# Performance work log

Hardware: AMD Instinct MI355X
Metric: run time of the kernel (lower is better)

## Reference

```python
import jax, jax.numpy as jnp
import numpy as np

B, H, S, D = 4, 32, 2048, 128  # batch, heads, seq_len, d_head
D_MODEL = H * D


def setup_inputs() -> dict:
    key = jax.random.key(0)
    ks = jax.random.split(key, 6)
    return {
        "query_states": jax.random.normal(ks[0], (B, H, S, D), dtype=jnp.float32),
        "key_states": jax.random.normal(ks[1], (B, H, S, D), dtype=jnp.float32),
        "value_states": jax.random.normal(ks[2], (B, H, S, D), dtype=jnp.float32),
        "local_attn_outputs": jax.random.normal(ks[3], (B, H, S, D), dtype=jnp.float32),
        "balance_factors": jax.random.normal(ks[4], (H,), dtype=jnp.float32),
        "w_o": jax.random.normal(ks[5], (D_MODEL, D_MODEL), dtype=jnp.float32) / np.sqrt(D_MODEL),
    }


def reference(query_states, key_states, value_states, local_attn_outputs, balance_factors, w_o):
    # --- compressive memory from keys/values (elu+1 feature map) ---
    phi_k = jax.nn.elu(key_states) + 1.0                                  # [B,H,S,D]
    memory = jnp.einsum("bhsk,bhsv->bhkv", phi_k, value_states)           # [B,H,D,D]
    normalization = jnp.sum(phi_k, axis=2)                                # [B,H,D]

    # --- retrieval with query feature map, normalized ---
    phi_q = jax.nn.elu(query_states) + 1.0                                # [B,H,S,D]
    retrieved = jnp.einsum("bhsk,bhkv->bhsv", phi_q, memory)              # [B,H,S,D]
    denom = jnp.einsum("bhsk,bhk->bhs", phi_q, normalization)             # [B,H,S]
    retrieved = retrieved / denom[..., None]

    # --- sigmoid-gated combine of global (memory) and local attention ---
    gw = jax.nn.sigmoid(balance_factors)[None, :, None, None]             # global weights
    lw = jax.nn.sigmoid(1.0 - balance_factors)[None, :, None, None]      # local weights
    attn = gw * retrieved + lw * local_attn_outputs                       # [B,H,S,D]

    # [B,H,S,D] -> [B,S,H*D]
    attn = jnp.transpose(attn, (0, 2, 1, 3)).reshape(B, S, H * D)
    # o_proj: bias-free Linear, y = x @ W^T
    return attn @ w_o.T
```

## Files before the change

### kernel.cpp

```cpp
#include <hip/hip_runtime.h>
#include <hip/hip_bf16.h>

#define B_ 4
#define H_ 32
#define S_ 2048
#define D_ 128
#define DM_ 4096
#define BH_ (B_*H_)
#define M_ (B_*S_)

typedef short bf16x8 __attribute__((ext_vector_type(8)));
typedef short s16x4  __attribute__((ext_vector_type(4)));
typedef float f32x4  __attribute__((ext_vector_type(4)));

__device__ __forceinline__ float phi_f(float x) {
    return x > 0.f ? x + 1.f : __expf(x);
}

__device__ __forceinline__ short f2b(float x) {
    __hip_bfloat16 h = __float2bfloat16(x);
    return *(short*)&h;
}

__device__ __forceinline__ void gl_lds16(void* lds_uniform, const void* gptr) {
    __builtin_amdgcn_global_load_lds(
        (const __attribute__((address_space(1))) void*)gptr,
        (__attribute__((address_space(3))) void*)lds_uniform,
        16, 0, 0);
}

__global__ __launch_bounds__(256) void k1_memory(
    const float* __restrict__ Kin, const float* __restrict__ Vin,
    float* __restrict__ memT, float* __restrict__ nrm)
{
    const int split = blockIdx.x;
    const int bh = blockIdx.y;
    const int t = threadIdx.x;
    const int wave = t >> 6, lane = t & 63;
    const int lm = lane & 15, quad = lane >> 4;
    const int wm = wave >> 1, wn = wave & 1;

    __shared__ __hip_bfloat16 sVt[128*72];
    __shared__ __hip_bfloat16 sKt[128*72];

    const long base = (long)bh * S_ * D_ + (long)split * (S_/4) * D_;
    const float* Kp = Kin + base;
    const float* Vp = Vin + base;

    f32x4 acc[4][4];
#pragma unroll
    for (int i = 0; i < 4; ++i)
#pragma unroll
        for (int j = 0; j < 4; ++j) { f32x4 z = {0.f,0.f,0.f,0.f}; acc[i][j] = z; }

    float na[2][4] = {{0.f,0.f,0.f,0.f},{0.f,0.f,0.f,0.f}};

    const int si  = t & 15;
    const int dj0 = t >> 4;

    for (int c = 0; c < 8; ++c) {
        const int s0 = c*64 + si*4;
        __syncthreads();
#pragma unroll
        for (int m = 0; m < 2; ++m) {
            const int dj = dj0 + 16*m;
            const float* gK = Kp + (long)s0*D_ + dj*4;
            const float* gV = Vp + (long)s0*D_ + dj*4;
            float4 krv[4], vrv[4];
#pragma unroll
            for (int r = 0; r < 4; ++r) {
                krv[r] = *(const float4*)(gK + (long)r*D_);
                vrv[r] = *(const float4*)(gV + (long)r*D_);
            }
            const float* kf = (const float*)krv;
            const float* vf = (const float*)vrv;
#pragma unroll
            for (int cc = 0; cc < 4; ++cc) {
                float p0 = phi_f(kf[0*4+cc]), p1 = phi_f(kf[1*4+cc]);
                float p2 = phi_f(kf[2*4+cc]), p3 = phi_f(kf[3*4+cc]);
                na[m][cc] += p0 + p1 + p2 + p3;
                s16x4 pw; pw[0]=f2b(p0); pw[1]=f2b(p1); pw[2]=f2b(p2); pw[3]=f2b(p3);
                s16x4 vw; vw[0]=f2b(vf[0*4+cc]); vw[1]=f2b(vf[1*4+cc]);
                          vw[2]=f2b(vf[2*4+cc]); vw[3]=f2b(vf[3*4+cc]);
                const int d = dj*4 + cc;
                *(s16x4*)(sKt + d*72 + si*4) = pw;
                *(s16x4*)(sVt + d*72 + si*4) = vw;
            }
        }
        __syncthreads();
#pragma unroll
        for (int kh = 0; kh < 2; ++kh) {
            const int scol = kh*32 + quad*8;
            bf16x8 af[4], bfr[4];
#pragma unroll
            for (int x = 0; x < 4; ++x) {
                af[x]  = *(const bf16x8*)(sVt + (wm*64 + x*16 + lm)*72 + scol);
                bfr[x] = *(const bf16x8*)(sKt + (wn*64 + x*16 + lm)*72 + scol);
            }
#pragma unroll
            for (int mt = 0; mt < 4; ++mt)
#pragma unroll
                for (int nt = 0; nt < 4; ++nt)
                    acc[mt][nt] = __builtin_amdgcn_mfma_f32_16x16x32_bf16(
                        af[mt], bfr[nt], acc[mt][nt], 0, 0, 0);
        }
    }

#pragma unroll
    for (int m = 0; m < 2; ++m)
#pragma unroll
        for (int cc = 0; cc < 4; ++cc) {
            float v = na[m][cc];
            v += __shfl_xor(v, 1); v += __shfl_xor(v, 2);
            v += __shfl_xor(v, 4); v += __shfl_xor(v, 8);
            if (si == 0)
                atomicAdd(&nrm[bh*D_ + (dj0 + 16*m)*4 + cc], v);
        }

    float* mp = memT + (long)bh * D_ * D_;
#pragma unroll
    for (int mt = 0; mt < 4; ++mt)
#pragma unroll
        for (int nt = 0; nt < 4; ++nt) {
            const int kcol = wn*64 + nt*16 + lm;
#pragma unroll
            for (int r = 0; r < 4; ++r) {
                const int vrow = wm*64 + mt*16 + quad*4 + r;
                atomicAdd(&mp[vrow*D_ + kcol], acc[mt][nt][r]);
            }
        }
}

__global__ __launch_bounds__(256) void k2_retrieve(
    const float* __restrict__ Qin, const float* __restrict__ Lin,
    const float* __restrict__ bal,
    const float* __restrict__ memT, const float* __restrict__ nrm,
    __hip_bfloat16* __restrict__ attnB)
{
    const int sc = blockIdx.x;
    const int bh = blockIdx.y;
    const int b = bh >> 5, h = bh & 31;
    const int t = threadIdx.x;
    const int wave = t >> 6, lane = t & 63;
    const int lm = lane & 15, quad = lane >> 4;
    const int wm = wave >> 1, wn = wave & 1;

    __shared__ __hip_bfloat16 sQ[128*128];
    __shared__ __hip_bfloat16 sM[128*128];
    __shared__ float sDen[128];

    const float* Qp = Qin + (long)bh*S_*D_ + (long)sc*128*D_;
    const float* Lp = Lin + (long)bh*S_*D_ + (long)sc*128*D_;
    const float* mp = memT + (long)bh*D_*D_;

    const int kq = t & 31;
    const float4 nq = *(const float4*)(nrm + bh*D_ + kq*4);

#pragma unroll
    for (int i = 0; i < 16; ++i) {
        const int idx = t + i*256;
        const int row = idx >> 5;
        float4 qv = *(const float4*)(Qp + (long)idx*4);
        float p0 = phi_f(qv.x), p1 = phi_f(qv.y), p2 = phi_f(qv.z), p3 = phi_f(qv.w);
        float part = p0*nq.x + p1*nq.y + p2*nq.z + p3*nq.w;
        part += __shfl_xor(part, 1);  part += __shfl_xor(part, 2);
        part += __shfl_xor(part, 4);  part += __shfl_xor(part, 8);
        part += __shfl_xor(part, 16);
        if (kq == 0) sDen[row] = part;
        const int seg = kq >> 1, half = kq & 1;
        const int off = row*128 + ((seg ^ (row & 15)) << 3) + half*4;
        s16x4 qw; qw[0]=f2b(p0); qw[1]=f2b(p1); qw[2]=f2b(p2); qw[3]=f2b(p3);
        *(s16x4*)(sQ + off) = qw;
        float4 mv = *(const float4*)(mp + (long)idx*4);
        s16x4 mw; mw[0]=f2b(mv.x); mw[1]=f2b(mv.y); mw[2]=f2b(mv.z); mw[3]=f2b(mv.w);
        *(s16x4*)(sM + off) = mw;
    }
    __syncthreads();

    f32x4 acc[4][4];
#pragma unroll
    for (int i = 0; i < 4; ++i)
#pragma unroll
        for (int j = 0; j < 4; ++j) { f32x4 z = {0.f,0.f,0.f,0.f}; acc[i][j] = z; }

#pragma unroll
    for (int kh = 0; kh < 4; ++kh) {
        const int segk = kh*4 + quad;
        bf16x8 af[4], bfr[4];
#pragma unroll
        for (int x = 0; x < 4; ++x) {
            const int srow = wm*64 + x*16 + lm;
            af[x]  = *(const bf16x8*)(sQ + srow*128 + ((segk ^ (srow & 15)) << 3));
            const int vrow = wn*64 + x*16 + lm;
            bfr[x] = *(const bf16x8*)(sM + vrow*128 + ((segk ^ (vrow & 15)) << 3));
        }
#pragma unroll
        for (int mt = 0; mt < 4; ++mt)
#pragma unroll
            for (int nt = 0; nt < 4; ++nt)
                acc[mt][nt] = __builtin_amdgcn_mfma_f32_16x16x32_bf16(
                    af[mt], bfr[nt], acc[mt][nt], 0, 0, 0);
    }

    const float bv = bal[h];
    const float gw = 1.f/(1.f+__expf(-bv));
    const float lw = 1.f/(1.f+__expf(-(1.f-bv)));
#pragma unroll
    for (int mt = 0; mt < 4; ++mt)
#pragma unroll
        for (int r = 0; r < 4; ++r) {
            const int srow = wm*64 + mt*16 + quad*4 + r;
            const float scale = gw / sDen[srow];
            const long orow = (long)b*S_ + sc*128 + srow;
#pragma unroll
            for (int nt = 0; nt < 4; ++nt) {
                const int vcol = wn*64 + nt*16 + lm;
                const float lvv = Lp[(long)srow*D_ + vcol];
                const float o = acc[mt][nt][r]*scale + lw*lvv;
                attnB[orow*DM_ + h*D_ + vcol] = __float2bfloat16(o);
            }
        }
}

__global__ __launch_bounds__(256) void kconv(
    const float* __restrict__ w, __hip_bfloat16* __restrict__ wb)
{
    long i = ((long)blockIdx.x*256 + threadIdx.x)*4;
    float4 f = *(const float4*)(w + i);
    __hip_bfloat16 ob[4] = {__float2bfloat16(f.x), __float2bfloat16(f.y),
                            __float2bfloat16(f.z), __float2bfloat16(f.w)};
    *(uint2*)(wb + i) = *(uint2*)ob;
}

#define GBM 256
#define GBN 256
#define GBK 64
#define GNT (DM_/GBK)

__device__ __forceinline__ bf16x8 ldfrag(const __hip_bfloat16* base, int row, int k) {
    const int kk = k ^ ((row & 7) << 3);
    return *(const bf16x8*)(base + row * GBK + kk);
}

__device__ __forceinline__ void stage_tile(
    const __hip_bfloat16* __restrict__ X, const __hip_bfloat16* __restrict__ W,
    __hip_bfloat16* sAb, __hip_bfloat16* sBb,
    int m0, int n0, int kb, int wave, int lane)
{
#pragma unroll
    for (int r = 0; r < 4; ++r) {
        const int c   = r * 512 + wave * 64 + lane;
        const int row = c >> 3;
        const int ko  = ((c & 7) ^ (row & 7)) * 8;
        gl_lds16((void*)(sAb + (r * 512 + wave * 64) * 8),
                 (const void*)(X + (long)(m0 + row) * DM_ + kb + ko));
    }
#pragma unroll
    for (int r = 0; r < 4; ++r) {
        const int c   = r * 512 + wave * 64 + lane;
        const int row = c >> 3;
        const int ko  = ((c & 7) ^ (row & 7)) * 8;
        gl_lds16((void*)(sBb + (r * 512 + wave * 64) * 8),
                 (const void*)(W + (long)(n0 + row) * DM_ + kb + ko));
    }
}

__global__ __launch_bounds__(512, 2) void k3_gemm(
    const __hip_bfloat16* __restrict__ X,
    const __hip_bfloat16* __restrict__ W,
    float* __restrict__ Y)
{
    __shared__ alignas(16) __hip_bfloat16 sA[2][GBM * GBK];
    __shared__ alignas(16) __hip_bfloat16 sB[2][GBN * GBK];

    const int tid = threadIdx.x;
    const int wave = tid >> 6, lane = tid & 63;
    const int lm = lane & 15, quad = lane >> 4;
    const int wm = wave >> 2, wn = wave & 3;

    const int orig = blockIdx.x;
    const int wg = (orig & 7) * 64 + (orig >> 3);
    const int m0 = (wg >> 4) * GBM;
    const int n0 = (wg & 15) * GBN;

    f32x4 acc[8][4];
#pragma unroll
    for (int i = 0; i < 8; ++i)
#pragma unroll
        for (int j = 0; j < 4; ++j) { f32x4 z = {0.f,0.f,0.f,0.f}; acc[i][j] = z; }

    const int ar0 = wm * 128 + lm;
    const int br0 = wn * 64 + lm;
    const int kq  = quad * 8;

    stage_tile(X, W, sA[0], sB[0], m0, n0, 0, wave, lane);
    stage_tile(X, W, sA[1], sB[1], m0, n0, GBK, wave, lane);
    asm volatile("s_waitcnt vmcnt(8)" ::: "memory");
    __builtin_amdgcn_s_barrier();

    bf16x8 a[4][2], b[4][2];

    for (int t = 0; t < GNT; ++t) {
        const int cur = t & 1;
        const __hip_bfloat16* As = sA[cur];
        const __hip_bfloat16* Bs = sB[cur];

#pragma unroll
        for (int mf = 0; mf < 4; ++mf)
#pragma unroll
            for (int kh = 0; kh < 2; ++kh)
                a[mf][kh] = ldfrag(As, ar0 + mf * 16, kh * 32 + kq);
#pragma unroll
        for (int nf = 0; nf < 2; ++nf)
#pragma unroll
            for (int kh = 0; kh < 2; ++kh)
                b[nf][kh] = ldfrag(Bs, br0 + nf * 16, kh * 32 + kq);
        __builtin_amdgcn_s_barrier();
        asm volatile("s_waitcnt lgkmcnt(0)" ::: "memory");
        __builtin_amdgcn_sched_barrier(0);
        __builtin_amdgcn_s_setprio(1);
#pragma unroll
        for (int mf = 0; mf < 4; ++mf)
#pragma unroll
            for (int nf = 0; nf < 2; ++nf)
#pragma unroll
                for (int kh = 0; kh < 2; ++kh)
                    acc[mf][nf] = __builtin_amdgcn_mfma_f32_16x16x32_bf16(
                        a[mf][kh], b[nf][kh], acc[mf][nf], 0, 0, 0);
        __builtin_amdgcn_s_setprio(0);
        __builtin_amdgcn_s_barrier();

#pragma unroll
        for (int nf = 2; nf < 4; ++nf)
#pragma unroll
            for (int kh = 0; kh < 2; ++kh)
                b[nf][kh] = ldfrag(Bs, br0 + nf * 16, kh * 32 + kq);
        __builtin_amdgcn_s_barrier();
        asm volatile("s_waitcnt lgkmcnt(0)" ::: "memory");
        __builtin_amdgcn_sched_barrier(0);
        __builtin_amdgcn_s_setprio(1);
#pragma unroll
        for (int mf = 0; mf < 4; ++mf)
#pragma unroll
            for (int nf = 2; nf < 4; ++nf)
#pragma unroll
                for (int kh = 0; kh < 2; ++kh)
                    acc[mf][nf] = __builtin_amdgcn_mfma_f32_16x16x32_bf16(
                        a[mf][kh], b[nf][kh], acc[mf][nf], 0, 0, 0);
        __builtin_amdgcn_s_setprio(0);
        __builtin_amdgcn_s_barrier();

#pragma unroll
        for (int mf = 0; mf < 4; ++mf)
#pragma unroll
            for (int kh = 0; kh < 2; ++kh)
                a[mf][kh] = ldfrag(As, ar0 + 64 + mf * 16, kh * 32 + kq);
        __builtin_amdgcn_s_barrier();
        asm volatile("s_waitcnt lgkmcnt(0)" ::: "memory");
        __builtin_amdgcn_sched_barrier(0);
        __builtin_amdgcn_s_setprio(1);
#pragma unroll
        for (int mf = 0; mf < 4; ++mf)
#pragma unroll
            for (int nf = 0; nf < 2; ++nf)
#pragma unroll
                for (int kh = 0; kh < 2; ++kh)
                    acc[4 + mf][nf] = __builtin_amdgcn_mfma_f32_16x16x32_bf16(
                        a[mf][kh], b[nf][kh], acc[4 + mf][nf], 0, 0, 0);
        __builtin_amdgcn_s_setprio(0);
        __builtin_amdgcn_s_barrier();

        if (t + 2 < GNT)
            stage_tile(X, W, sA[cur], sB[cur], m0, n0, (t + 2) * GBK, wave, lane);
        __builtin_amdgcn_s_barrier();
        __builtin_amdgcn_s_setprio(1);
#pragma unroll
        for (int mf = 0; mf < 4; ++mf)
#pragma unroll
            for (int nf = 2; nf < 4; ++nf)
#pragma unroll
                for (int kh = 0; kh < 2; ++kh)
                    acc[4 + mf][nf] = __builtin_amdgcn_mfma_f32_16x16x32_bf16(
                        a[mf][kh], b[nf][kh], acc[4 + mf][nf], 0, 0, 0);
        __builtin_amdgcn_s_setprio(0);
        if (t + 2 < GNT)
            asm volatile("s_waitcnt vmcnt(8)" ::: "memory");
        else
            asm volatile("s_waitcnt vmcnt(0)" ::: "memory");
        __builtin_amdgcn_s_barrier();
    }

#pragma unroll
    for (int mf = 0; mf < 8; ++mf) {
        const int row = m0 + wm * 128 + mf * 16 + quad * 4;
#pragma unroll
        for (int nf = 0; nf < 4; ++nf) {
            const int col = n0 + wn * 64 + nf * 16 + lm;
#pragma unroll
            for (int r = 0; r < 4; ++r)
                Y[(long)(row + r) * DM_ + col] = acc[mf][nf][r];
        }
    }
}

extern "C" void kernel_launch(void* const* d_in, const int* in_sizes, int n_in,
                              void* d_out, int out_size, void* d_ws, size_t ws_size,
                              hipStream_t stream) {
    const float* Q   = (const float*)d_in[0];
    const float* K   = (const float*)d_in[1];
    const float* V   = (const float*)d_in[2];
    const float* L   = (const float*)d_in[3];
    const float* bal = (const float*)d_in[4];
    const float* Wo  = (const float*)d_in[5];
    float* Y = (float*)d_out;

    char* ws = (char*)d_ws;
    float* memT  = (float*)ws;
    float* norm  = (float*)(ws + 8388608);
    __hip_bfloat16* attnB = (__hip_bfloat16*)(ws + 8454144);
    __hip_bfloat16* woB   = (__hip_bfloat16*)(ws + 75563008);

    hipMemsetAsync(memT, 0, 8454144, stream);

    k1_memory<<<dim3(4, BH_), 256, 0, stream>>>(K, V, memT, norm);
    kconv<<<DM_*DM_/4/256, 256, 0, stream>>>(Wo, woB);
    k2_retrieve<<<dim3(S_/128, BH_), 256, 0, stream>>>(Q, L, bal, memT, norm, attnB);
    k3_gemm<<<dim3(512), 512, 0, stream>>>(attnB, woB, Y);
}
```

Baseline: 888.6 us.

## Replace memory atomics with split partials, bf16 finalize, and coalesced retrieve epilogue

k1 now writes per-split partial memory matrices with plain stores instead of float atomics, and a new finalize kernel sums the four splits and writes a pre-swizzled bf16 memory matrix. k2 loads that bf16 matrix straight into LDS with global_load_lds, so every tile no longer re-reads and converts the fp32 matrix. k2's epilogue now stages results in LDS and writes attn output and reads the local outputs with wide coalesced accesses, replacing the scattered scalar accesses. The cost is an extra kernel launch and a larger partials buffer in the workspace, which overlaps woB because kconv runs after finalize.

```diff
diff --git a/kernel.cpp b/kernel.cpp
--- a/kernel.cpp
+++ b/kernel.cpp
@@ -31,7 +31,7 @@
 
 __global__ __launch_bounds__(256) void k1_memory(
     const float* __restrict__ Kin, const float* __restrict__ Vin,
-    float* __restrict__ memT, float* __restrict__ nrm)
+    float* __restrict__ parts, float* __restrict__ nrm)
 {
     const int split = blockIdx.x;
     const int bh = blockIdx.y;
@@ -117,7 +117,7 @@
                 atomicAdd(&nrm[bh*D_ + (dj0 + 16*m)*4 + cc], v);
         }
 
-    float* mp = memT + (long)bh * D_ * D_;
+    float* mp = parts + ((long)split*BH_ + bh) * (D_*D_);
 #pragma unroll
     for (int mt = 0; mt < 4; ++mt)
 #pragma unroll
@@ -126,15 +126,38 @@
 #pragma unroll
             for (int r = 0; r < 4; ++r) {
                 const int vrow = wm*64 + mt*16 + quad*4 + r;
-                atomicAdd(&mp[vrow*D_ + kcol], acc[mt][nt][r]);
+                mp[vrow*D_ + kcol] = acc[mt][nt][r];
             }
         }
+}
+
+__global__ __launch_bounds__(256) void k1b_finalize(
+    const float* __restrict__ parts, __hip_bfloat16* __restrict__ memTb)
+{
+    const long g = (long)blockIdx.x*256 + threadIdx.x;
+    const int bh  = (int)(g >> 11);
+    const int rem = (int)(g & 2047);
+    const int row = rem >> 4, seg = rem & 15;
+    const int srcSeg = seg ^ (row & 15);
+    const long sbase = (long)bh*(D_*D_) + row*D_ + srcSeg*8;
+
+    f32x4 s0 = {0.f,0.f,0.f,0.f}, s1 = {0.f,0.f,0.f,0.f};
+#pragma unroll
+    for (int sp = 0; sp < 4; ++sp) {
+        const float* p = parts + (long)sp*BH_*(D_*D_) + sbase;
+        s0 += *(const f32x4*)p;
+        s1 += *(const f32x4*)(p + 4);
+    }
+    bf16x8 ob;
+#pragma unroll
+    for (int j = 0; j < 4; ++j) { ob[j] = f2b(s0[j]); ob[4+j] = f2b(s1[j]); }
+    *(bf16x8*)(memTb + g*8) = ob;
 }
 
 __global__ __launch_bounds__(256) void k2_retrieve(
     const float* __restrict__ Qin, const float* __restrict__ Lin,
     const float* __restrict__ bal,
-    const float* __restrict__ memT, const float* __restrict__ nrm,
+    const __hip_bfloat16* __restrict__ memTb, const float* __restrict__ nrm,
     __hip_bfloat16* __restrict__ attnB)
 {
     const int sc = blockIdx.x;
@@ -145,17 +168,23 @@
     const int lm = lane & 15, quad = lane >> 4;
     const int wm = wave >> 1, wn = wave & 1;
 
-    __shared__ __hip_bfloat16 sQ[128*128];
-    __shared__ __hip_bfloat16 sM[128*128];
+    __shared__ char smem[128*132*4];
+    __hip_bfloat16* sQ = (__hip_bfloat16*)smem;
+    __hip_bfloat16* sM = (__hip_bfloat16*)(smem + 32768);
+    float* sOut = (float*)smem;
     __shared__ float sDen[128];
 
     const float* Qp = Qin + (long)bh*S_*D_ + (long)sc*128*D_;
     const float* Lp = Lin + (long)bh*S_*D_ + (long)sc*128*D_;
-    const float* mp = memT + (long)bh*D_*D_;
+    const __hip_bfloat16* mb = memTb + (long)bh*(D_*D_);
+
+#pragma unroll
+    for (int i = 0; i < 8; ++i)
+        gl_lds16((void*)(sM + (i*256 + wave*64)*8),
+                 (const void*)(mb + (long)(i*256 + wave*64 + lane)*8));
 
     const int kq = t & 31;
     const float4 nq = *(const float4*)(nrm + bh*D_ + kq*4);
-
 #pragma unroll
     for (int i = 0; i < 16; ++i) {
         const int idx = t + i*256;
@@ -171,9 +200,6 @@
         const int off = row*128 + ((seg ^ (row & 15)) << 3) + half*4;
         s16x4 qw; qw[0]=f2b(p0); qw[1]=f2b(p1); qw[2]=f2b(p2); qw[3]=f2b(p3);
         *(s16x4*)(sQ + off) = qw;
-        float4 mv = *(const float4*)(mp + (long)idx*4);
-        s16x4 mw; mw[0]=f2b(mv.x); mw[1]=f2b(mv.y); mw[2]=f2b(mv.z); mw[3]=f2b(mv.w);
-        *(s16x4*)(sM + off) = mw;
     }
     __syncthreads();
 
@@ -205,21 +231,38 @@
     const float bv = bal[h];
     const float gw = 1.f/(1.f+__expf(-bv));
     const float lw = 1.f/(1.f+__expf(-(1.f-bv)));
+
+    __syncthreads();
 #pragma unroll
     for (int mt = 0; mt < 4; ++mt)
 #pragma unroll
         for (int r = 0; r < 4; ++r) {
             const int srow = wm*64 + mt*16 + quad*4 + r;
             const float scale = gw / sDen[srow];
-            const long orow = (long)b*S_ + sc*128 + srow;
-#pragma unroll
-            for (int nt = 0; nt < 4; ++nt) {
-                const int vcol = wn*64 + nt*16 + lm;
-                const float lvv = Lp[(long)srow*D_ + vcol];
-                const float o = acc[mt][nt][r]*scale + lw*lvv;
-                attnB[orow*DM_ + h*D_ + vcol] = __float2bfloat16(o);
-            }
-        }
+#pragma unroll
+            for (int nt = 0; nt < 4; ++nt)
+                sOut[srow*132 + wn*64 + nt*16 + lm] = acc[mt][nt][r]*scale;
+        }
+    __syncthreads();
+
+    const int seg = t & 15;
+#pragma unroll
+    for (int i = 0; i < 8; ++i) {
+        const int row = (t >> 4) + i*16;
+        const float* Lr = Lp + (long)row*D_ + seg*8;
+        const float* Or = sOut + row*132 + seg*8;
+        float4 l0 = *(const float4*)Lr;
+        float4 l1 = *(const float4*)(Lr + 4);
+        f32x4 o0 = *(const f32x4*)Or;
+        f32x4 o1 = *(const f32x4*)(Or + 4);
+        bf16x8 ob;
+        ob[0] = f2b(o0[0] + lw*l0.x); ob[1] = f2b(o0[1] + lw*l0.y);
+        ob[2] = f2b(o0[2] + lw*l0.z); ob[3] = f2b(o0[3] + lw*l0.w);
+        ob[4] = f2b(o1[0] + lw*l1.x); ob[5] = f2b(o1[1] + lw*l1.y);
+        ob[6] = f2b(o1[2] + lw*l1.z); ob[7] = f2b(o1[3] + lw*l1.w);
+        const long oidx = ((long)b*S_ + sc*128 + row)*DM_ + h*D_ + seg*8;
+        *(bf16x8*)(attnB + oidx) = ob;
+    }
 }
 
 __global__ __launch_bounds__(256) void kconv(
@@ -415,15 +458,17 @@
     float* Y = (float*)d_out;
 
     char* ws = (char*)d_ws;
-    float* memT  = (float*)ws;
-    float* norm  = (float*)(ws + 8388608);
-    __hip_bfloat16* attnB = (__hip_bfloat16*)(ws + 8454144);
-    __hip_bfloat16* woB   = (__hip_bfloat16*)(ws + 75563008);
-
-    hipMemsetAsync(memT, 0, 8454144, stream);
-
-    k1_memory<<<dim3(4, BH_), 256, 0, stream>>>(K, V, memT, norm);
+    float* parts = (float*)ws;
+    __hip_bfloat16* woB = (__hip_bfloat16*)ws;
+    float* nrm   = (float*)(ws + 33554432);
+    __hip_bfloat16* memTb = (__hip_bfloat16*)(ws + 33619968);
+    __hip_bfloat16* attnB = (__hip_bfloat16*)(ws + 37814272);
+
+    hipMemsetAsync(nrm, 0, 65536, stream);
+
+    k1_memory<<<dim3(4, BH_), 256, 0, stream>>>(K, V, parts, nrm);
+    k1b_finalize<<<1024, 256, 0, stream>>>(parts, memTb);
     kconv<<<DM_*DM_/4/256, 256, 0, stream>>>(Wo, woB);
-    k2_retrieve<<<dim3(S_/128, BH_), 256, 0, stream>>>(Q, L, bal, memT, norm, attnB);
+    k2_retrieve<<<dim3(S_/128, BH_), 256, 0, stream>>>(Q, L, bal, memTb, nrm, attnB);
     k3_gemm<<<dim3(512), 512, 0, stream>>>(attnB, woB, Y);
 }
```

After: 889.6 us. Within noise of the previous version (+0.1%).
